# Kernel optimization log

Hardware: AMD Instinct MI355X
Metric: run time of the kernel (lower is better)

## Reference

```python
import jax, jax.numpy as jnp
import numpy as np

Q_DIM = 2048
HEADS = 16
HEAD_DIM = 128
INNER = HEADS * HEAD_DIM          # 2048
MLP_HID = int(Q_DIM * 4.0)        # 8192
MLP_MULT = 2
EPS = 1e-05
B, S = 2, 2048


def setup_inputs() -> dict:
    key = jax.random.key(0)
    ks = jax.random.split(key, 4)
    hidden_states = jax.random.normal(ks[0], (B, S, Q_DIM), dtype=jnp.float32)
    # interleaved RoPE tables: cos/sin of shape [S, HEAD_DIM]
    half = HEAD_DIM // 2
    freqs = 1.0 / (10000.0 ** (np.arange(half, dtype=np.float64) / half))
    ang = np.outer(np.arange(S, dtype=np.float64), freqs)      # [S, half]
    ang = np.repeat(ang, 2, axis=-1)                            # [S, HEAD_DIM]
    rope_cos = jnp.asarray(np.cos(ang), dtype=jnp.float32)
    rope_sin = jnp.asarray(np.sin(ang), dtype=jnp.float32)
    fused_out = 3 * INNER + MLP_HID * MLP_MULT                  # 22528
    W_qkv_mlp = jax.random.normal(ks[1], (Q_DIM, fused_out), dtype=jnp.float32) * (Q_DIM ** -0.5)
    norm_q_w = jnp.ones((HEAD_DIM,), dtype=jnp.float32)
    norm_k_w = jnp.ones((HEAD_DIM,), dtype=jnp.float32)
    W_out = jax.random.normal(ks[2], (INNER + MLP_HID, Q_DIM), dtype=jnp.float32) * ((INNER + MLP_HID) ** -0.5)
    b_out = jnp.zeros((Q_DIM,), dtype=jnp.float32)
    return {"hidden_states": hidden_states, "rope_cos": rope_cos, "rope_sin": rope_sin,
            "W_qkv_mlp": W_qkv_mlp, "norm_q_w": norm_q_w, "norm_k_w": norm_k_w,
            "W_out": W_out, "b_out": b_out}


def _rms_norm(x, w):
    # RMSNorm over the last (head_dim) axis
    return x * jax.lax.rsqrt(jnp.mean(x * x, axis=-1, keepdims=True) + EPS) * w


def _apply_rope(x, cos, sin):
    # x: [B, S, H, D]; interleaved rotate-half (diffusers real-rope convention)
    xr = x.reshape(*x.shape[:-1], HEAD_DIM // 2, 2)
    rot = jnp.stack([-xr[..., 1], xr[..., 0]], axis=-1).reshape(x.shape)
    return x * cos[None, :, None, :] + rot * sin[None, :, None, :]


def reference(hidden_states, rope_cos, rope_sin, W_qkv_mlp, norm_q_w, norm_k_w, W_out, b_out):
    b, s, _ = hidden_states.shape
    proj = hidden_states @ W_qkv_mlp                              # [B,S,22528]
    qkv, mlp_h = jnp.split(proj, [3 * INNER], axis=-1)
    q, k, v = jnp.split(qkv, 3, axis=-1)
    q = q.reshape(b, s, HEADS, HEAD_DIM)
    k = k.reshape(b, s, HEADS, HEAD_DIM)
    v = v.reshape(b, s, HEADS, HEAD_DIM)
    q = _rms_norm(q, norm_q_w)
    k = _rms_norm(k, norm_k_w)
    q = _apply_rope(q, rope_cos, rope_sin)
    k = _apply_rope(k, rope_cos, rope_sin)
    scale = HEAD_DIM ** -0.5
    scores = jnp.einsum('bqhd,bkhd->bhqk', q, k) * scale          # [B,H,S,S]
    attn = jax.nn.softmax(scores, axis=-1)
    out_attn = jnp.einsum('bhqk,bkhd->bqhd', attn, v).reshape(b, s, INNER)
    m1, m2 = jnp.split(mlp_h, 2, axis=-1)                         # SwiGLU
    mlp_out = jax.nn.silu(m1) * m2                                # [B,S,MLP_HID]
    cat = jnp.concatenate([out_attn, mlp_out], axis=-1)           # [B,S,INNER+MLP_HID]
    return cat @ W_out + b_out
```

## Files before the change

kernel.cpp:

```cpp
#include <hip/hip_runtime.h>

typedef unsigned short u16;
typedef unsigned int u32;
typedef __bf16 bf16x8 __attribute__((ext_vector_type(8)));
typedef float f32x4 __attribute__((ext_vector_type(4)));

#define MFMA16(a, b, c) __builtin_amdgcn_mfma_f32_16x16x32_bf16((a), (b), (c), 0, 0, 0)

#define S_LEN 2048
#define D_HEAD 128
#define NHEADS 16
#define NBH 32
#define QDIM 2048
#define NPROJ 22528
#define NQKV 6144
#define NMLP 16384
#define NCAT 10240
#define MROWS 4096

#define BARRIER() __builtin_amdgcn_s_barrier()
#define WAITVM0() asm volatile("s_waitcnt vmcnt(0)" ::: "memory")

__device__ __forceinline__ float bf2f(u16 u) { return __uint_as_float(((u32)u) << 16); }
__device__ __forceinline__ u16 f2bf(float f) {
  u32 u = __float_as_uint(f);
  return (u16)((u + 0x7FFFu + ((u >> 16) & 1u)) >> 16);
}
__device__ __forceinline__ void gld16(const void* g, void* l) {
  __builtin_amdgcn_global_load_lds((__attribute__((address_space(1))) void*)(g),
                                   (__attribute__((address_space(3))) void*)(l), 16, 0, 0);
}

__global__ __launch_bounds__(256) void f32_to_bf16(const float* __restrict__ in,
                                                   u16* __restrict__ out) {
  const u32 i = blockIdx.x * 256 + threadIdx.x;
  const float4 v = ((const float4*)in)[i];
  uint2 o;
  o.x = (u32)f2bf(v.x) | ((u32)f2bf(v.y) << 16);
  o.y = (u32)f2bf(v.z) | ((u32)f2bf(v.w) << 16);
  ((uint2*)out)[i] = o;
}

template <int REMAP>
__global__ __launch_bounds__(256) void transpose_f32_bf16(const float* __restrict__ in,
                                                          u16* __restrict__ out, int R, int C) {
  __shared__ u16 tile[64][260];
  const int t = threadIdx.x;
  const int tx = t & 63;
  const int ty = t >> 6;
  const int c0 = blockIdx.x * 64;
  const int r0 = blockIdx.y * 256;

#pragma unroll 8
  for (int it = 0; it < 64; ++it) {
    const int rr = it * 4 + ty;
    tile[tx][rr] = f2bf(in[(size_t)(r0 + rr) * C + c0 + tx]);
  }
  __syncthreads();

  const int pos = t & 63;
#pragma unroll 4
  for (int i = 0; i < 16; ++i) {
    const int cc = i * 4 + (t >> 6);
    int orow = c0 + cc;
    if (REMAP && orow >= NQKV) {
      const int c = orow - NQKV;
      const int f = c & 8191;
      const int sel = c >> 13;
      orow = NQKV + (((f >> 4) << 5) | (sel << 4) | (f & 15));
    }
    const u32 lo = (u32)tile[cc][pos * 4] | ((u32)tile[cc][pos * 4 + 1] << 16);
    const u32 hi = (u32)tile[cc][pos * 4 + 2] | ((u32)tile[cc][pos * 4 + 3] << 16);
    uint2 v;
    v.x = lo;
    v.y = hi;
    *(uint2*)&out[(size_t)orow * R + r0 + pos * 4] = v;
  }
}

template <int OUTMODE>
__global__ __launch_bounds__(256, 2) void gemm_bt(const u16* __restrict__ A,
                                                  const u16* __restrict__ Bt,
                                                  void* __restrict__ Cvoid,
                                                  const float* __restrict__ bias, int N, int K) {
  __shared__ u16 As[128 * 64];
  __shared__ u16 Bs[128 * 64];
  const int t = threadIdx.x;
  const int l = t & 63;
  const int w = t >> 6;
  const int lr = l & 15;
  const int lg = l >> 4;
  const int m0 = blockIdx.y * 128;
  const int n0 = blockIdx.x * 128;
  const int wm = (w >> 1) * 64;
  const int wn = (w & 1) * 64;

  f32x4 acc[4][4] = {};
  const int obase = w * 1024 + l * 16;

  for (int k0 = 0; k0 < K; k0 += 64) {
#pragma unroll
    for (int rnd = 0; rnd < 4; ++rnd) {
      const int o = obase + rnd * 4096;
      const int row = o >> 7;
      const int g = (o & 127) >> 4;
      const int gs = g ^ (row & 7);
      gld16(A + (size_t)(m0 + row) * K + k0 + gs * 8, &As[rnd * 2048 + w * 512]);
      gld16(Bt + (size_t)(n0 + row) * K + k0 + gs * 8, &Bs[rnd * 2048 + w * 512]);
    }
    __syncthreads();

    bf16x8 af[4][2], bfr[4][2];
#pragma unroll
    for (int i = 0; i < 4; ++i) {
#pragma unroll
      for (int kc = 0; kc < 2; ++kc) {
        const int ra = wm + i * 16 + lr;
        af[i][kc] = *(const bf16x8*)&As[ra * 64 + (((kc * 4 + lg) ^ (ra & 7)) * 8)];
        const int rb = wn + i * 16 + lr;
        bfr[i][kc] = *(const bf16x8*)&Bs[rb * 64 + (((kc * 4 + lg) ^ (rb & 7)) * 8)];
      }
    }
#pragma unroll
    for (int kc = 0; kc < 2; ++kc)
#pragma unroll
      for (int i = 0; i < 4; ++i)
#pragma unroll
        for (int j = 0; j < 4; ++j)
          acc[i][j] = MFMA16(af[i][kc], bfr[j][kc], acc[i][j]);
    __syncthreads();
  }

  if (OUTMODE == 1) {
    float* C = (float*)Cvoid;
#pragma unroll
    for (int i = 0; i < 4; ++i)
#pragma unroll
      for (int j = 0; j < 4; ++j)
#pragma unroll
        for (int r = 0; r < 4; ++r) {
          const int row = m0 + wm + i * 16 + lg * 4 + r;
          const int col = n0 + wn + j * 16 + lr;
          C[(size_t)row * N + col] = acc[i][j][r] + bias[col];
        }
  } else {
    u16* C = (u16*)Cvoid;
#pragma unroll
    for (int i = 0; i < 4; ++i)
#pragma unroll
      for (int jj = 0; jj < 2; ++jj)
#pragma unroll
        for (int r = 0; r < 4; ++r) {
          const int row = m0 + wm + i * 16 + lg * 4 + r;
          const float a1 = acc[i][2 * jj][r];
          const float a2 = acc[i][2 * jj + 1][r];
          const float fz = a1 / (1.f + __expf(-a1)) * a2;
          const int col = ((n0 + wn) >> 1) + jj * 16 + lr;
          C[(size_t)row * N + col] = f2bf(fz);
        }
  }
}

__global__ __launch_bounds__(256, 2) void gemm_qkv(const u16* __restrict__ A,
                                                   const u16* __restrict__ Bt,
                                                   const float* __restrict__ cosT,
                                                   const float* __restrict__ sinT,
                                                   const float* __restrict__ wq,
                                                   const float* __restrict__ wk,
                                                   u16* __restrict__ Qb, u16* __restrict__ Kb,
                                                   u16* __restrict__ Vt, int K) {
  __shared__ u16 smem[2][128 * 64];
  __shared__ float redbuf[2][128];
  u16* As = smem[0];
  u16* Bs = smem[1];
  const int t = threadIdx.x;
  const int l = t & 63;
  const int w = t >> 6;
  const int lr = l & 15;
  const int lg = l >> 4;
  const int m0 = blockIdx.y * 128;
  const int n0 = blockIdx.x * 128;
  const int wm = (w >> 1) * 64;
  const int wn = (w & 1) * 64;

  f32x4 acc[4][4] = {};
  const int obase = w * 1024 + l * 16;

  for (int k0 = 0; k0 < K; k0 += 64) {
#pragma unroll
    for (int rnd = 0; rnd < 4; ++rnd) {
      const int o = obase + rnd * 4096;
      const int row = o >> 7;
      const int g = (o & 127) >> 4;
      const int gs = g ^ (row & 7);
      gld16(A + (size_t)(m0 + row) * K + k0 + gs * 8, As + rnd * 2048 + w * 512);
      gld16(Bt + (size_t)(n0 + row) * K + k0 + gs * 8, Bs + rnd * 2048 + w * 512);
    }
    __syncthreads();

    bf16x8 af[4][2], bfr[4][2];
#pragma unroll
    for (int i = 0; i < 4; ++i) {
#pragma unroll
      for (int kc = 0; kc < 2; ++kc) {
        const int ra = wm + i * 16 + lr;
        af[i][kc] = *(const bf16x8*)&As[ra * 64 + (((kc * 4 + lg) ^ (ra & 7)) * 8)];
        const int rb = wn + i * 16 + lr;
        bfr[i][kc] = *(const bf16x8*)&Bs[rb * 64 + (((kc * 4 + lg) ^ (rb & 7)) * 8)];
      }
    }
#pragma unroll
    for (int kc = 0; kc < 2; ++kc)
#pragma unroll
      for (int i = 0; i < 4; ++i)
#pragma unroll
        for (int j = 0; j < 4; ++j)
          acc[i][j] = MFMA16(af[i][kc], bfr[j][kc], acc[i][j]);
    __syncthreads();
  }

  const int type = n0 >> 11;
  const int h = (n0 >> 7) & 15;
  const int b = m0 >> 11;
  const int s0 = m0 & 2047;
  const int bh = b * 16 + h;

  if (type == 2) {
    u16* vt = smem[0];
#pragma unroll
    for (int i = 0; i < 4; ++i)
#pragma unroll
      for (int j = 0; j < 4; ++j)
#pragma unroll
        for (int r = 0; r < 4; ++r) {
          const int s_loc = wm + i * 16 + lg * 4 + r;
          const int d = wn + j * 16 + lr;
          vt[d * 128 + (s_loc ^ ((d & 7) << 3))] = f2bf(acc[i][j][r]);
        }
    __syncthreads();
    const int g = t & 15;
#pragma unroll
    for (int i = 0; i < 8; ++i) {
      const int d2 = i * 16 + (t >> 4);
      const bf16x8 v = *(const bf16x8*)&vt[d2 * 128 + ((g ^ (d2 & 7)) * 8)];
      *(bf16x8*)&Vt[((size_t)(bh * 128 + d2)) * S_LEN + s0 + g * 8] = v;
    }
    return;
  }

  u16* dst = (type == 0) ? Qb : Kb;

  float ssum[4][4];
#pragma unroll
  for (int i = 0; i < 4; ++i)
#pragma unroll
    for (int r = 0; r < 4; ++r) {
      float p = acc[i][0][r] * acc[i][0][r] + acc[i][1][r] * acc[i][1][r] +
                acc[i][2][r] * acc[i][2][r] + acc[i][3][r] * acc[i][3][r];
      p += __shfl_xor(p, 1);
      p += __shfl_xor(p, 2);
      p += __shfl_xor(p, 4);
      p += __shfl_xor(p, 8);
      ssum[i][r] = p;
    }
  if (lr == 0) {
#pragma unroll
    for (int i = 0; i < 4; ++i)
#pragma unroll
      for (int r = 0; r < 4; ++r) redbuf[wn >> 6][wm + i * 16 + lg * 4 + r] = ssum[i][r];
  }
  __syncthreads();

  const float* wgt = type ? wk : wq;
  const float sc = type ? 1.0f : 0.12751744f;
#pragma unroll
  for (int i = 0; i < 4; ++i)
#pragma unroll
    for (int r = 0; r < 4; ++r) {
      const int lrow = wm + i * 16 + lg * 4 + r;
      const float tot = redbuf[0][lrow] + redbuf[1][lrow];
      const float rsq = rsqrtf(tot * (1.0f / 128.0f) + 1e-5f) * sc;
      const int s = (m0 + lrow) & 2047;
      const size_t rbase = ((size_t)bh * S_LEN + s) * 128;
#pragma unroll
      for (int j = 0; j < 4; ++j) {
        const int col = wn + j * 16 + lr;
        const float xn = acc[i][j][r] * rsq * wgt[col];
        const float pr = __shfl_xor(xn, 1);
        const float c = cosT[s * 128 + col];
        const float sn = sinT[s * 128 + col];
        const float val = (col & 1) ? (xn * c + pr * sn) : (xn * c - pr * sn);
        dst[rbase + col] = f2bf(val);
      }
    }
}

__global__ __launch_bounds__(256, 2) void attn_fwd(const u16* __restrict__ Qb,
                                                   const u16* __restrict__ Kb,
                                                   const u16* __restrict__ Vt,
                                                   u16* __restrict__ Cat) {
  __shared__ u16 Ks[2][64 * 128];
  __shared__ u16 Vs[2][128 * 64];
  __shared__ u16 Ps[4][32 * 64];

  const int t = threadIdx.x;
  const int l = t & 63;
  const int w = t >> 6;
  const int lr = l & 15;
  const int lg = l >> 4;
  const int swz = (blockIdx.x & 7) * 64 + (blockIdx.x >> 3);
  const int qt = swz & 15;
  const int bh = swz >> 4;
  const int b = bh >> 4;
  const int h = bh & 15;
  const int q0 = qt * 128 + w * 32;
  const int obase = w * 1024 + l * 16;

  const size_t kbase = (size_t)bh * S_LEN * 128;
  const size_t vbase = (size_t)bh * 128 * S_LEN;

  bf16x8 qf[2][4];
#pragma unroll
  for (int im = 0; im < 2; ++im)
#pragma unroll
    for (int kc = 0; kc < 4; ++kc)
      qf[im][kc] =
          *(const bf16x8*)&Qb[((size_t)bh * S_LEN + q0 + im * 16 + lr) * 128 + kc * 32 + lg * 8];

  f32x4 oacc[2][8] = {};
  float lrun[2][4] = {};

  u16* P = Ps[w];

  auto stageKV = [&](int buf, int kt2) {
    const int kk0 = kt2 * 64;
#pragma unroll
    for (int rnd = 0; rnd < 4; ++rnd) {
      const int o = obase + rnd * 4096;
      {
        const int key = o >> 8;
        const int g = (o & 255) >> 4;
        const int gs = g ^ (key & 7);
        gld16(Kb + kbase + (size_t)(kk0 + key) * 128 + gs * 8,
              &Ks[buf][rnd * 2048 + w * 512]);
      }
      {
        const int d = o >> 7;
        const int g = (o & 127) >> 4;
        const int gs = g ^ (d & 7);
        gld16(Vt + vbase + (size_t)d * S_LEN + kk0 + gs * 8,
              &Vs[buf][rnd * 2048 + w * 512]);
      }
    }
  };

  stageKV(0, 0);
  WAITVM0();
  BARRIER();

  int cur = 0;
  for (int kt = 0; kt < 32; ++kt) {
    if (kt + 1 < 32) stageKV(cur ^ 1, kt + 1);

    const u16* Kc = &Ks[cur][0];
    const u16* Vc = &Vs[cur][0];

    f32x4 sf[2][4] = {};
    __builtin_amdgcn_s_setprio(1);
#pragma unroll
    for (int j = 0; j < 4; ++j) {
      const int kr = j * 16 + lr;
      bf16x8 kf[4];
#pragma unroll
      for (int kc = 0; kc < 4; ++kc)
        kf[kc] = *(const bf16x8*)&Kc[kr * 128 + (((kc * 4 + lg) ^ (kr & 7)) * 8)];
#pragma unroll
      for (int kc = 0; kc < 4; ++kc)
#pragma unroll
        for (int im = 0; im < 2; ++im)
          sf[im][j] = MFMA16(qf[im][kc], kf[kc], sf[im][j]);
    }
    __builtin_amdgcn_s_setprio(0);

#pragma unroll
    for (int im = 0; im < 2; ++im)
#pragma unroll
      for (int r = 0; r < 4; ++r) {
        float psum = 0.f;
#pragma unroll
        for (int j = 0; j < 4; ++j) {
          const float pv = exp2f(sf[im][j][r]);
          sf[im][j][r] = pv;
          psum += pv;
        }
        lrun[im][r] += psum;
      }

#pragma unroll
    for (int im = 0; im < 2; ++im)
#pragma unroll
      for (int j = 0; j < 4; ++j)
#pragma unroll
        for (int r = 0; r < 4; ++r) {
          const int q = im * 16 + lg * 4 + r;
          const int key = j * 16 + lr;
          const int g = key >> 3;
          P[q * 64 + ((g ^ (q & 7)) * 8) + (key & 7)] = f2bf(sf[im][j][r]);
        }

    __builtin_amdgcn_s_setprio(1);
#pragma unroll
    for (int kc = 0; kc < 2; ++kc) {
      bf16x8 pa[2];
#pragma unroll
      for (int im = 0; im < 2; ++im) {
        const int q = im * 16 + lr;
        pa[im] = *(const bf16x8*)&P[q * 64 + (((kc * 4 + lg) ^ (q & 7)) * 8)];
      }
#pragma unroll
      for (int df = 0; df < 8; ++df) {
        const int d = df * 16 + lr;
        const bf16x8 vb = *(const bf16x8*)&Vc[d * 64 + (((kc * 4 + lg) ^ (d & 7)) * 8)];
#pragma unroll
        for (int im = 0; im < 2; ++im) oacc[im][df] = MFMA16(pa[im], vb, oacc[im][df]);
      }
    }
    __builtin_amdgcn_s_setprio(0);

    WAITVM0();
    BARRIER();
    cur ^= 1;
  }

#pragma unroll
  for (int im = 0; im < 2; ++im)
#pragma unroll
    for (int r = 0; r < 4; ++r) {
      float tot = lrun[im][r];
      tot += __shfl_xor(tot, 1);
      tot += __shfl_xor(tot, 2);
      tot += __shfl_xor(tot, 4);
      tot += __shfl_xor(tot, 8);
      const float inv = 1.0f / tot;
      const int row = b * S_LEN + q0 + im * 16 + lg * 4 + r;
#pragma unroll
      for (int df = 0; df < 8; ++df) {
        const int col = h * 128 + df * 16 + lr;
        Cat[(size_t)row * NCAT + col] = f2bf(oacc[im][df][r] * inv);
      }
    }
}

extern "C" void kernel_launch(void* const* d_in, const int* in_sizes, int n_in, void* d_out,
                              int out_size, void* d_ws, size_t ws_size, hipStream_t stream) {
  (void)in_sizes; (void)n_in; (void)out_size; (void)ws_size;
  const float* hs = (const float*)d_in[0];
  const float* rcos = (const float*)d_in[1];
  const float* rsin = (const float*)d_in[2];
  const float* Wqkv = (const float*)d_in[3];
  const float* wq = (const float*)d_in[4];
  const float* wk = (const float*)d_in[5];
  const float* Wout = (const float*)d_in[6];
  const float* bout = (const float*)d_in[7];
  float* out = (float*)d_out;

  char* ws = (char*)d_ws;
  size_t off = 0;
  auto nxt = [&](size_t bytes) {
    char* p = ws + off;
    off += (bytes + 255) & ~(size_t)255;
    return p;
  };
  u16* Xb = (u16*)nxt((size_t)MROWS * QDIM * 2);
  u16* Wqkvt = (u16*)nxt((size_t)NPROJ * QDIM * 2);
  u16* Woutt = (u16*)nxt((size_t)QDIM * NCAT * 2);
  u16* Qb = (u16*)nxt((size_t)NBH * S_LEN * D_HEAD * 2);
  u16* Kb = (u16*)nxt((size_t)NBH * S_LEN * D_HEAD * 2);
  u16* Vt = (u16*)nxt((size_t)NBH * S_LEN * D_HEAD * 2);
  u16* Cat = (u16*)nxt((size_t)MROWS * NCAT * 2);

  f32_to_bf16<<<(MROWS * QDIM / 4) / 256, 256, 0, stream>>>(hs, Xb);
  transpose_f32_bf16<1><<<dim3(NPROJ / 64, QDIM / 256), 256, 0, stream>>>(Wqkv, Wqkvt, QDIM,
                                                                          NPROJ);
  transpose_f32_bf16<0><<<dim3(QDIM / 64, NCAT / 256), 256, 0, stream>>>(Wout, Woutt, NCAT,
                                                                         QDIM);

  gemm_qkv<<<dim3(NQKV / 128, MROWS / 128), 256, 0, stream>>>(Xb, Wqkvt, rcos, rsin, wq, wk,
                                                              Qb, Kb, Vt, QDIM);
  gemm_bt<2><<<dim3(NMLP / 128, MROWS / 128), 256, 0, stream>>>(
      Xb, Wqkvt + (size_t)NQKV * QDIM, Cat + QDIM, nullptr, NCAT, QDIM);

  attn_fwd<<<S_LEN / 128 * NBH, 256, 0, stream>>>(Qb, Kb, Vt, Cat);

  gemm_bt<1><<<dim3(QDIM / 128, MROWS / 128), 256, 0, stream>>>(Cat, Woutt, out, bout, QDIM,
                                                                NCAT);
}
```

Measured before the change: 769.1 us.

## Add 256x256 multi-stage pipelined MLP GEMM kernel with SwiGLU epilogue

Replaces the 128x128 MLP projection GEMM with a dedicated 512-thread kernel that computes 256x256 tiles, using a 4-deep LDS ring buffer of K=32 slices loaded via global_load_lds. Loads are issued three stages ahead, and register-level ping-pong of B fragments plus s_setprio overlap MFMA with LDS reads. The aim is higher arithmetic intensity and latency hiding for the largest GEMM. The cost is one block per CU, heavy register use, and a fragile manual vmcnt/barrier schedule. The generic gemm_bt template is simplified to only its fp32 bias output mode.

```diff
diff --git a/kernel.cpp b/kernel.cpp
--- a/kernel.cpp
+++ b/kernel.cpp
@@ -19,7 +19,9 @@
 #define MROWS 4096
 
 #define BARRIER() __builtin_amdgcn_s_barrier()
+#define FENCE() asm volatile("" ::: "memory")
 #define WAITVM0() asm volatile("s_waitcnt vmcnt(0)" ::: "memory")
+#define WAITVM4() asm volatile("s_waitcnt vmcnt(4)" ::: "memory")
 
 __device__ __forceinline__ float bf2f(u16 u) { return __uint_as_float(((u32)u) << 16); }
 __device__ __forceinline__ u16 f2bf(float f) {
@@ -78,10 +80,125 @@
   }
 }
 
-template <int OUTMODE>
+
+__device__ __forceinline__ void stage32(const u16* __restrict__ src, int K, int base,
+                                        u16* dst, int k0, int t) {
+#pragma unroll
+  for (int jj = 0; jj < 2; ++jj) {
+    const int o = (jj * 512 + t) * 16;
+    const int pr = o >> 7;
+    const int gs = (o & 127) >> 4;
+    const int ga = gs ^ (pr & 7);
+    const int row = pr * 2 + (ga >> 2);
+    const int k8 = ga & 3;
+    gld16(src + (size_t)(base + row) * K + k0 + k8 * 8,
+          dst + (jj * 512 + (t & ~63)) * 8);
+  }
+}
+
+__device__ __forceinline__ bf16x8 rd32(const u16* buf, int row, int lg) {
+  const int pr = row >> 1;
+  const int ga = ((row & 1) << 2) | lg;
+  const int gs = ga ^ (pr & 7);
+  return *(const bf16x8*)&buf[pr * 64 + gs * 8];
+}
+
+#define ITER(KT, BCUR, BNXT)                                                        \
+  {                                                                                 \
+    const int d_ = (KT) & 3, dn_ = ((KT) + 1) & 3, ds_ = ((KT) + 3) & 3;            \
+                                  \
+    _Pragma("unroll") for (int i = 0; i < 4; ++i)                                   \
+        aB[i] = rd32(&As[d_][0], wm + 64 + i * 16 + lr, lg);                        \
+    if ((KT) + 3 < NT) stage32(A, K, m0, &As[ds_][0], ((KT) + 3) * 32, t);          \
+    BARRIER();                                                                      \
+    FENCE();                                                                        \
+    __builtin_amdgcn_s_setprio(1);                                                  \
+    _Pragma("unroll") for (int i = 0; i < 4; ++i)                                   \
+    _Pragma("unroll") for (int j = 0; j < 4; ++j)                                   \
+        acc[i][j] = MFMA16(aA[i], BCUR[j], acc[i][j]);                              \
+    __builtin_amdgcn_s_setprio(0);                                                  \
+    BARRIER();                                                                      \
+    FENCE();                                                                        \
+                         \
+    if ((KT) + 1 < NT) {                                                            \
+      _Pragma("unroll") for (int i = 0; i < 4; ++i)                                 \
+          aA[i] = rd32(&As[dn_][0], wm + i * 16 + lr, lg);                          \
+      _Pragma("unroll") for (int j = 0; j < 4; ++j)                                 \
+          BNXT[j] = rd32(&Bs[dn_][0], wn + j * 16 + lr, lg);                        \
+    }                                                                               \
+    if ((KT) + 3 < NT) stage32(Bt, K, n0, &Bs[ds_][0], ((KT) + 3) * 32, t);         \
+    BARRIER();                                                                      \
+    FENCE();                                                                        \
+    __builtin_amdgcn_s_setprio(1);                                                  \
+    _Pragma("unroll") for (int i = 0; i < 4; ++i)                                   \
+    _Pragma("unroll") for (int j = 0; j < 4; ++j)                                   \
+        acc[4 + i][j] = MFMA16(aB[i], BCUR[j], acc[4 + i][j]);                      \
+    __builtin_amdgcn_s_setprio(0);                                                  \
+    if ((KT) >= NT - 4) {                                                           \
+      WAITVM0();                                                                    \
+    } else {                                                                        \
+      WAITVM4();                                                                    \
+    }                                                                               \
+    BARRIER();                                                                      \
+    FENCE();                                                                        \
+  }
+
+__global__ __launch_bounds__(512, 1) void gemm_mlp(const u16* __restrict__ A,
+                                                   const u16* __restrict__ Bt,
+                                                   u16* __restrict__ Cat, int K) {
+  __shared__ u16 As[4][256 * 32];
+  __shared__ u16 Bs[4][256 * 32];
+  const int t = threadIdx.x;
+  const int l = t & 63;
+  const int w = t >> 6;
+  const int lr = l & 15;
+  const int lg = l >> 4;
+  const int m0 = blockIdx.y * 256;
+  const int n0 = blockIdx.x * 256;
+  const int wm = (w >> 2) * 128;
+  const int wn = (w & 3) * 64;
+  const int NT = K >> 5;
+
+  f32x4 acc[8][4] = {};
+  bf16x8 aA[4], aB[4], bC[4], bD[4];
+
+  stage32(A, K, m0, &As[0][0], 0, t);
+  stage32(Bt, K, n0, &Bs[0][0], 0, t);
+  stage32(A, K, m0, &As[1][0], 32, t);
+  stage32(Bt, K, n0, &Bs[1][0], 32, t);
+  stage32(A, K, m0, &As[2][0], 64, t);
+  stage32(Bt, K, n0, &Bs[2][0], 64, t);
+  WAITVM4();
+  BARRIER();
+  FENCE();
+#pragma unroll
+  for (int i = 0; i < 4; ++i) aA[i] = rd32(&As[0][0], wm + i * 16 + lr, lg);
+#pragma unroll
+  for (int j = 0; j < 4; ++j) bC[j] = rd32(&Bs[0][0], wn + j * 16 + lr, lg);
+
+  for (int kt = 0; kt < NT; kt += 2) {
+    ITER(kt, bC, bD)
+    ITER(kt + 1, bD, bC)
+  }
+
+#pragma unroll
+  for (int i = 0; i < 8; ++i)
+#pragma unroll
+    for (int jj = 0; jj < 2; ++jj)
+#pragma unroll
+      for (int r = 0; r < 4; ++r) {
+        const int row = m0 + wm + i * 16 + lg * 4 + r;
+        const float a1 = acc[i][2 * jj][r];
+        const float a2 = acc[i][2 * jj + 1][r];
+        const float fz = a1 / (1.f + __expf(-a1)) * a2;
+        const int col = ((n0 + wn) >> 1) + jj * 16 + lr;
+        Cat[(size_t)row * NCAT + col] = f2bf(fz);
+      }
+}
+
 __global__ __launch_bounds__(256, 2) void gemm_bt(const u16* __restrict__ A,
                                                   const u16* __restrict__ Bt,
-                                                  void* __restrict__ Cvoid,
+                                                  float* __restrict__ C,
                                                   const float* __restrict__ bias, int N, int K) {
   __shared__ u16 As[128 * 64];
   __shared__ u16 Bs[128 * 64];
@@ -131,34 +248,16 @@
     __syncthreads();
   }
 
-  if (OUTMODE == 1) {
-    float* C = (float*)Cvoid;
-#pragma unroll
-    for (int i = 0; i < 4; ++i)
-#pragma unroll
-      for (int j = 0; j < 4; ++j)
-#pragma unroll
-        for (int r = 0; r < 4; ++r) {
-          const int row = m0 + wm + i * 16 + lg * 4 + r;
-          const int col = n0 + wn + j * 16 + lr;
-          C[(size_t)row * N + col] = acc[i][j][r] + bias[col];
-        }
-  } else {
-    u16* C = (u16*)Cvoid;
-#pragma unroll
-    for (int i = 0; i < 4; ++i)
-#pragma unroll
-      for (int jj = 0; jj < 2; ++jj)
-#pragma unroll
-        for (int r = 0; r < 4; ++r) {
-          const int row = m0 + wm + i * 16 + lg * 4 + r;
-          const float a1 = acc[i][2 * jj][r];
-          const float a2 = acc[i][2 * jj + 1][r];
-          const float fz = a1 / (1.f + __expf(-a1)) * a2;
-          const int col = ((n0 + wn) >> 1) + jj * 16 + lr;
-          C[(size_t)row * N + col] = f2bf(fz);
-        }
-  }
+#pragma unroll
+  for (int i = 0; i < 4; ++i)
+#pragma unroll
+    for (int j = 0; j < 4; ++j)
+#pragma unroll
+      for (int r = 0; r < 4; ++r) {
+        const int row = m0 + wm + i * 16 + lg * 4 + r;
+        const int col = n0 + wn + j * 16 + lr;
+        C[(size_t)row * N + col] = acc[i][j][r] + bias[col];
+      }
 }
 
 __global__ __launch_bounds__(256, 2) void gemm_qkv(const u16* __restrict__ A,
@@ -487,11 +586,11 @@
 
   gemm_qkv<<<dim3(NQKV / 128, MROWS / 128), 256, 0, stream>>>(Xb, Wqkvt, rcos, rsin, wq, wk,
                                                               Qb, Kb, Vt, QDIM);
-  gemm_bt<2><<<dim3(NMLP / 128, MROWS / 128), 256, 0, stream>>>(
-      Xb, Wqkvt + (size_t)NQKV * QDIM, Cat + QDIM, nullptr, NCAT, QDIM);
+  gemm_mlp<<<dim3(NMLP / 256, MROWS / 256), 512, 0, stream>>>(
+      Xb, Wqkvt + (size_t)NQKV * QDIM, Cat + QDIM, QDIM);
 
   attn_fwd<<<S_LEN / 128 * NBH, 256, 0, stream>>>(Qb, Kb, Vt, Cat);
 
-  gemm_bt<1><<<dim3(QDIM / 128, MROWS / 128), 256, 0, stream>>>(Cat, Woutt, out, bout, QDIM,
-                                                                NCAT);
-}
+  gemm_bt<<<dim3(QDIM / 128, MROWS / 128), 256, 0, stream>>>(Cat, Woutt, out, bout, QDIM,
+                                                             NCAT);
+}
```

Measured after the change: 790.0 us. 2.7% more time.
